# Performance work log

Hardware: AMD Instinct MI355X
Metric: run time of the kernel (lower is better)

Reference implementation:

```python
import jax, jax.numpy as jnp
import numpy as np

B, T, L, E, H, QS = 8, 8, 197, 768, 12, 16
C = E // H


def setup_inputs() -> dict:
    key = jax.random.key(0)
    ks = jax.random.split(key, 10)
    return dict(
        x=jax.random.normal(ks[0], (B, T, L, E), jnp.float32) * 0.02,
        s=jax.random.normal(ks[1], (B, QS, E), jnp.float32) * 0.02,
        te=jax.random.normal(ks[2], (T, E), jnp.float32) * 0.02,
        patch_mask=jax.random.normal(ks[3], (B, T, 1, L - 1, 1), jnp.float32) * 0.02,
        in_proj_weight=jax.random.normal(ks[4], (3 * E, E), jnp.float32) * 0.02,
        in_proj_bias=jax.random.normal(ks[5], (3 * E,), jnp.float32) * 0.02,
        out_w=jax.random.normal(ks[6], (E, E), jnp.float32) * 0.02,
        out_b=jax.random.normal(ks[7], (E,), jnp.float32) * 0.02,
        conv_w=jax.random.normal(ks[8], (E, 1, 3), jnp.float32) * 0.001,  # depthwise, groups=E
        conv_b=jax.random.normal(ks[9], (E,), jnp.float32) * 0.02,
    )


def _qkv(z, w, b, head_shape):
    # F.linear(z, w, b).chunk(3, -1), each reshaped to (*head_shape, H, C)
    zz = z @ w.T + b
    q, k, v = jnp.split(zz, 3, axis=-1)
    return (q.reshape(*head_shape, H, C),
            k.reshape(*head_shape, H, C),
            v.reshape(*head_shape, H, C))


def reference(x, s, te, patch_mask, in_proj_weight, in_proj_bias, out_w, out_b, conv_w, conv_b):
    scale = 1.0 / jnp.sqrt(jnp.asarray(C, x.dtype))

    # main self-attention over patches, per frame
    q, k, v = _qkv(x, in_proj_weight, in_proj_bias, (B, T, L))
    aff = jnp.einsum('ntqhc,ntkhc->ntqkh', q * scale, k)
    aff = jax.nn.softmax(aff, axis=-2)  # softmax over key dim (dim=-2)
    mix = jnp.einsum('ntqlh,ntlhc->ntqhc', aff, v)
    out = mix.reshape(B, T, L, E) @ out_w.T + out_b

    # syno cross-attention stream
    s_q, s_k, s_v = _qkv(s, in_proj_weight, in_proj_bias, (B, QS))
    te_q, te_k, te_v = _qkv(te, in_proj_weight, in_proj_bias, (T, 1))  # [T,1,H,C]
    _k = k[:, :, 1:]  # drop CLS -> [B,T,L-1,H,C]
    _v = v[:, :, 1:]
    s_aff = jnp.einsum('nqhc,ntkhc->ntqkh', s_q * scale, _k + te_k)
    s_aff = s_aff + patch_mask
    s_aff = jax.nn.softmax(s_aff, axis=-2)
    s_mix = jnp.einsum('ntqlh,ntlhc->ntqhc', s_aff, _v + te_v)  # [B,T,QS,H,C]

    # depthwise temporal conv (kernel 3, pad 1, groups=E) with residual
    sm = s_mix.transpose(0, 2, 3, 4, 1).reshape(B * QS, E, T)  # [N*Q, E, T]
    conv = jax.lax.conv_general_dilated(
        sm, conv_w, window_strides=(1,), padding=((1, 1),),
        feature_group_count=E, dimension_numbers=('NCH', 'OIH', 'NCH'))
    sm = conv + conv_b[None, :, None] + sm
    s_mix = sm.reshape(B, QS, H, C, T).transpose(0, 4, 1, 2, 3)  # [B,T,QS,H,C]

    s_mix = s_mix.mean(axis=1)  # mean over frames -> [B,QS,H,C]
    s_out = s_mix.reshape(B, QS, E) @ out_w.T + out_b

    return (q, k, v, out, s_q, s_k, s_v, s_out)
```

## Files before the change

### kernel.cpp

```cpp
#include <hip/hip_runtime.h>
#include <math.h>

constexpr int Bb  = 8;
constexpr int Tt  = 8;
constexpr int Ll  = 197;
constexpr int Ee  = 768;
constexpr int Hh  = 12;
constexpr int QSs = 16;
constexpr int Cc  = 64;
constexpr int MX    = Bb * Tt * Ll;
constexpr int MS    = Bb * QSs;
constexpr int MTE   = Tt;
constexpr int MALL  = MX + MS + MTE;
constexpr int MPAD  = 12800;
constexpr int KkP = 224;

using f32x4 = __attribute__((ext_vector_type(4))) float;
using s16x8 = __attribute__((ext_vector_type(8))) short;

__device__ __forceinline__ unsigned short f2bf(float f) {
    unsigned int u = __float_as_uint(f);
    u = (u + 0x7fffu + ((u >> 16) & 1u)) >> 16;
    return (unsigned short)u;
}

__global__ __launch_bounds__(256) void convert_all(
    const float* __restrict__ x, const float* __restrict__ s,
    const float* __restrict__ te, const float* __restrict__ ipw,
    const float* __restrict__ ow, unsigned short* __restrict__ xb,
    unsigned short* __restrict__ wb, unsigned short* __restrict__ owb)
{
    const long oX  = (long)MX * Ee;
    const long oS  = oX + (long)MS * Ee;
    const long oTe = oS + (long)MTE * Ee;
    const long nXp = (long)MPAD * Ee;
    const long nW  = (long)3 * Ee * Ee;
    const long nOW = (long)Ee * Ee;
    const long i4 = ((long)blockIdx.x * 256 + threadIdx.x) * 4;

    const float* src = nullptr; unsigned short* dst; long off, soff = 0;
    if (i4 < nXp) {
        dst = xb; off = i4;
        if      (off < oX)  { src = x;  soff = off; }
        else if (off < oS)  { src = s;  soff = off - oX; }
        else if (off < oTe) { src = te; soff = off - oS; }
    } else if (i4 < nXp + nW) {
        dst = wb; off = i4 - nXp; src = ipw; soff = off;
    } else if (i4 < nXp + nW + nOW) {
        dst = owb; off = i4 - nXp - nW; src = ow; soff = off;
    } else return;

    float4 v = make_float4(0.f, 0.f, 0.f, 0.f);
    if (src) v = *reinterpret_cast<const float4*>(src + soff);
    ushort4 o;
    o.x = f2bf(v.x); o.y = f2bf(v.y); o.z = f2bf(v.z); o.w = f2bf(v.w);
    *reinterpret_cast<ushort4*>(dst + off) = o;
}

struct DstPtrs { float* d[9]; };

__device__ __forceinline__ void load_lds16(const unsigned short* g, unsigned short* l) {
    __builtin_amdgcn_global_load_lds(
        (const __attribute__((address_space(1))) unsigned int*)g,
        (__attribute__((address_space(3))) unsigned int*)l,
        16, 0, 0);
}

__global__ __launch_bounds__(256) void mfma_gemm(
    const unsigned short* __restrict__ A,
    const unsigned short* __restrict__ W,
    const float* __restrict__ bias,
    DstPtrs dp, int Mmain, int Ms, int Mte,
    int ntiles, int tilesPerSeg)
{
    __shared__ __align__(16) unsigned short Asm[128 * 32];
    __shared__ __align__(16) unsigned short Bsm[128 * 32];

    const int nwg = gridDim.x;
    const int bid = blockIdx.x;
    const int q8 = nwg >> 3, r8 = nwg & 7;
    const int xcd = bid & 7, pos = bid >> 3;
    const int wgid = (xcd < r8 ? xcd * (q8 + 1)
                               : r8 * (q8 + 1) + (xcd - r8) * q8) + pos;
    const int mtile = wgid / ntiles;
    const int ntile = wgid - mtile * ntiles;

    const int tid  = threadIdx.x;
    const int wave = tid >> 6;
    const int lane = tid & 63;
    const int wr = wave >> 1, wc = wave & 1;
    const int m0  = mtile * 128;
    const int seg = ntile / tilesPerSeg;
    const int n0g = (ntile % tilesPerSeg) * 128;
    const int n0w = ntile * 128;

    f32x4 acc[4][4];
#pragma unroll
    for (int i = 0; i < 4; ++i)
#pragma unroll
        for (int j = 0; j < 4; ++j)
            acc[i][j] = f32x4{0.f, 0.f, 0.f, 0.f};

    const int srow = tid >> 2;
    const int scol = (tid & 3) * 8;
    unsigned short* ldsA = Asm + ((size_t)(tid >> 6)) * 512;
    unsigned short* ldsB = Bsm + ((size_t)(tid >> 6)) * 512;

    const int frow = lane & 15;
    const int fkc  = (lane >> 4) * 8;

    for (int k0 = 0; k0 < 768; k0 += 32) {
#pragma unroll
        for (int it = 0; it < 2; ++it) {
            const unsigned short* ga = A + (size_t)(m0 + srow + it * 64) * 768 + k0 + scol;
            const unsigned short* gb = W + (size_t)(n0w + srow + it * 64) * 768 + k0 + scol;
            load_lds16(ga, ldsA + it * 2048);
            load_lds16(gb, ldsB + it * 2048);
        }
        __syncthreads();

        s16x8 af[4], bf[4];
#pragma unroll
        for (int i = 0; i < 4; ++i) {
            const int ar = wr * 64 + i * 16 + frow;
            af[i] = *reinterpret_cast<const s16x8*>(&Asm[ar * 32 + fkc]);
        }
#pragma unroll
        for (int j = 0; j < 4; ++j) {
            const int br = wc * 64 + j * 16 + frow;
            bf[j] = *reinterpret_cast<const s16x8*>(&Bsm[br * 32 + fkc]);
        }
#pragma unroll
        for (int i = 0; i < 4; ++i)
#pragma unroll
            for (int j = 0; j < 4; ++j)
                acc[i][j] = __builtin_amdgcn_mfma_f32_16x16x32_bf16(
                    af[i], bf[j], acc[i][j], 0, 0, 0);
        __syncthreads();
    }

#pragma unroll
    for (int j = 0; j < 4; ++j) {
        const int col = wc * 64 + j * 16 + (lane & 15);
        const float bv = bias[n0w + col];
#pragma unroll
        for (int i = 0; i < 4; ++i) {
            const int gmBase = m0 + wr * 64 + i * 16 + ((lane >> 4) << 2);
            float* base; int lr;
            if (gmBase < Mmain)                { base = dp.d[seg];     lr = gmBase; }
            else if (gmBase < Mmain + Ms)      { base = dp.d[3 + seg]; lr = gmBase - Mmain; }
            else if (gmBase < Mmain + Ms + Mte){ base = dp.d[6 + seg]; lr = gmBase - Mmain - Ms; }
            else continue;
            float* p = base + (size_t)lr * 768 + n0g + col;
#pragma unroll
            for (int r = 0; r < 4; ++r)
                p[(size_t)r * 768] = acc[i][j][r] + bv;
        }
    }
}

__global__ __launch_bounds__(256) void attn_mfma(
    const float* __restrict__ q, const float* __restrict__ k,
    const float* __restrict__ v, unsigned short* __restrict__ mixb)
{
    __shared__ __align__(16) unsigned short Ks[KkP * 64];
    __shared__ __align__(16) unsigned short Vt[64 * 256];
    __shared__ __align__(16) unsigned short Pb[4 * 16 * 256];

    const int bidx = blockIdx.x;
    const int h  = bidx % Hh;
    const int bt = bidx / Hh;
    const int tid  = threadIdx.x;
    const int wave = tid >> 6;
    const int lane = tid & 63;
    const int l15  = lane & 15;
    const int g    = lane >> 4;
    const size_t gbase = (size_t)bt * Ll * Ee + (size_t)h * Cc;

    for (int idx = tid; idx < KkP * 16; idx += 256) {
        const int row = idx >> 4;
        const int cg  = idx & 15;
        float4 kv = make_float4(0.f, 0.f, 0.f, 0.f);
        if (row < Ll)
            kv = *reinterpret_cast<const float4*>(k + gbase + (size_t)row * Ee + cg * 4);
        ushort4 kb; kb.x = f2bf(kv.x); kb.y = f2bf(kv.y); kb.z = f2bf(kv.z); kb.w = f2bf(kv.w);
        const int kbyte = (row * 128 + cg * 8) ^ ((row & 7) << 4);
        *reinterpret_cast<ushort4*>((char*)Ks + kbyte) = kb;
    }
    for (int idx = tid; idx < 112 * 16; idx += 256) {
        const int rp = idx >> 4;
        const int cg = idx & 15;
        const int r0 = rp * 2, r1 = rp * 2 + 1;
        float4 v0 = make_float4(0.f, 0.f, 0.f, 0.f);
        float4 v1 = make_float4(0.f, 0.f, 0.f, 0.f);
        if (r0 < Ll) v0 = *reinterpret_cast<const float4*>(v + gbase + (size_t)r0 * Ee + cg * 4);
        if (r1 < Ll) v1 = *reinterpret_cast<const float4*>(v + gbase + (size_t)r1 * Ee + cg * 4);
        const float a0[4] = {v0.x, v0.y, v0.z, v0.w};
        const float a1[4] = {v1.x, v1.y, v1.z, v1.w};
#pragma unroll
        for (int i = 0; i < 4; ++i) {
            const int c = cg * 4 + i;
            const unsigned int w = (unsigned)f2bf(a0[i]) | ((unsigned)f2bf(a1[i]) << 16);
            const int vbyte = (c * 512 + rp * 4) ^ ((c & 7) << 4);
            *reinterpret_cast<unsigned int*>((char*)Vt + vbyte) = w;
        }
    }
    __syncthreads();

    char* Pw = (char*)(Pb + wave * 16 * 256);

    for (int qt = wave; qt < 13; qt += 4) {
        const int qrow = qt * 16 + l15;
        const float* qp = q + gbase + (size_t)qrow * Ee;
        s16x8 qf[2];
#pragma unroll
        for (int ks = 0; ks < 2; ++ks) {
            float4 a = make_float4(0.f, 0.f, 0.f, 0.f);
            float4 b = make_float4(0.f, 0.f, 0.f, 0.f);
            if (qrow < Ll) {
                a = *reinterpret_cast<const float4*>(qp + ks * 32 + g * 8);
                b = *reinterpret_cast<const float4*>(qp + ks * 32 + g * 8 + 4);
            }
            qf[ks] = s16x8{(short)f2bf(a.x), (short)f2bf(a.y), (short)f2bf(a.z), (short)f2bf(a.w),
                           (short)f2bf(b.x), (short)f2bf(b.y), (short)f2bf(b.z), (short)f2bf(b.w)};
        }

        float lsq = 0.f;
        for (int kt = 0; kt < 14; ++kt) {
            const int krow = kt * 16 + l15;
            f32x4 acc = {0.f, 0.f, 0.f, 0.f};
#pragma unroll
            for (int ks = 0; ks < 2; ++ks) {
                const int byte = (krow * 128 + ks * 64 + g * 16) ^ ((krow & 7) << 4);
                const s16x8 kf = *reinterpret_cast<const s16x8*>((const char*)Ks + byte);
                acc = __builtin_amdgcn_mfma_f32_16x16x32_bf16(kf, qf[ks], acc, 0, 0, 0);
            }
            float p[4];
#pragma unroll
            for (int r = 0; r < 4; ++r) {
                const int kg = kt * 16 + g * 4 + r;
                p[r] = (kg < Ll) ? __expf(acc[r] * 0.125f) : 0.f;
                lsq += p[r];
            }
            const unsigned int w0 = (unsigned)f2bf(p[0]) | ((unsigned)f2bf(p[1]) << 16);
            const unsigned int w1 = (unsigned)f2bf(p[2]) | ((unsigned)f2bf(p[3]) << 16);
            const int k0 = kt * 16 + g * 4;
            const int pbyte = (l15 * 512 + k0 * 2) ^ ((l15 & 7) << 4);
            *reinterpret_cast<unsigned int*>(Pw + pbyte)     = w0;
            *reinterpret_cast<unsigned int*>(Pw + pbyte + 4) = w1;
        }
        lsq += __shfl_xor(lsq, 16);
        lsq += __shfl_xor(lsq, 32);
        const float invl = 1.f / lsq;

#pragma unroll
        for (int ct = 0; ct < 4; ++ct) {
            f32x4 acc = {0.f, 0.f, 0.f, 0.f};
#pragma unroll
            for (int ks = 0; ks < 7; ++ks) {
                const int pbyte = (l15 * 512 + ks * 64 + g * 16) ^ ((l15 & 7) << 4);
                const s16x8 pf = *reinterpret_cast<const s16x8*>(Pw + pbyte);
                const int crow = ct * 16 + l15;
                const int vbyte = (crow * 512 + ks * 64 + g * 16) ^ ((crow & 7) << 4);
                const s16x8 vf = *reinterpret_cast<const s16x8*>((const char*)Vt + vbyte);
                acc = __builtin_amdgcn_mfma_f32_16x16x32_bf16(pf, vf, acc, 0, 0, 0);
            }
#pragma unroll
            for (int r = 0; r < 4; ++r) {
                const int qw = g * 4 + r;
                const float iv = __shfl(invl, qw);
                const int qg = qt * 16 + qw;
                if (qg < Ll) {
                    mixb[(size_t)(bt * Ll + qg) * Ee + h * Cc + ct * 16 + l15] =
                        f2bf(acc[r] * iv);
                }
            }
        }
    }
}

__global__ __launch_bounds__(256) void s_attn_v3(
    const float* __restrict__ sq, const float* __restrict__ k,
    const float* __restrict__ v, const float* __restrict__ tek,
    const float* __restrict__ tev, const float* __restrict__ pmask,
    float* __restrict__ smix)
{
    __shared__ float Ks[196][68];
    __shared__ float P[16][200];
    __shared__ float pm[196];
    __shared__ float teks[64];

    const int bt = blockIdx.x;
    const int h  = blockIdx.y;
    const int b  = bt / Tt;
    const int tt = bt % Tt;
    const int tid = threadIdx.x;
    const int qi = tid >> 4;
    const int kl = tid & 15;

    const size_t kbase = (size_t)bt * Ll * Ee + (size_t)h * Cc;
    for (int idx = tid; idx < 196 * 16; idx += 256) {
        const int row = idx >> 4;
        const int cg  = (idx & 15) * 4;
        *reinterpret_cast<float4*>(&Ks[row][cg]) =
            *reinterpret_cast<const float4*>(k + kbase + (size_t)(row + 1) * Ee + cg);
    }
    if (tid < 64) teks[tid] = tek[tt * Ee + h * Cc + tid];
    for (int i = tid; i < 196; i += 256)
        pm[i] = pmask[(size_t)bt * 196 + i];
    __syncthreads();

    float qr[Cc];
    const size_t sqbase = ((size_t)(b * QSs + qi)) * Ee + (size_t)h * Cc;
#pragma unroll
    for (int c4 = 0; c4 < 16; ++c4) {
        const float4 qv = *reinterpret_cast<const float4*>(sq + sqbase + c4 * 4);
        qr[c4*4+0] = qv.x; qr[c4*4+1] = qv.y; qr[c4*4+2] = qv.z; qr[c4*4+3] = qv.w;
    }
    float qte = 0.f;
#pragma unroll
    for (int c = 0; c < Cc; ++c) qte += qr[c] * teks[c];

    float lsum = 0.f;
    for (int i = 0; i < 13; ++i) {
        const int kk = kl + 16 * i;
        if (kk < 196) {
            float d = 0.f;
#pragma unroll
            for (int c4 = 0; c4 < 16; ++c4) {
                const float4 kv = *reinterpret_cast<const float4*>(&Ks[kk][c4 * 4]);
                d += qr[c4*4+0]*kv.x + qr[c4*4+1]*kv.y + qr[c4*4+2]*kv.z + qr[c4*4+3]*kv.w;
            }
            const float p = __expf((d + qte) * 0.125f + pm[kk]);
            P[qi][kk] = p;
            lsum += p;
        }
    }
    lsum += __shfl_xor(lsum, 1);
    lsum += __shfl_xor(lsum, 2);
    lsum += __shfl_xor(lsum, 4);
    lsum += __shfl_xor(lsum, 8);
    const float invl = 1.f / lsum;
    __syncthreads();

    const int c = kl * 4;
    const float4 tv = *reinterpret_cast<const float4*>(tev + tt * Ee + h * Cc + c);
    float a0 = 0.f, a1 = 0.f, a2 = 0.f, a3 = 0.f;
    const float* vbase = v + kbase + Ee + c;
    for (int kk = 0; kk < 196; ++kk) {
        const float p = P[qi][kk];
        const float4 vv = *reinterpret_cast<const float4*>(vbase + (size_t)kk * Ee);
        a0 += p * vv.x; a1 += p * vv.y; a2 += p * vv.z; a3 += p * vv.w;
    }
    float4 o;
    o.x = a0 * invl + tv.x; o.y = a1 * invl + tv.y;
    o.z = a2 * invl + tv.z; o.w = a3 * invl + tv.w;
    *reinterpret_cast<float4*>(
        smix + ((size_t)(bt * QSs + qi)) * Ee + (size_t)h * Cc + c) = o;
}

__global__ __launch_bounds__(256) void conv_mean_kernel(
    const float* __restrict__ smix, const float* __restrict__ cw,
    const float* __restrict__ cb, unsigned short* __restrict__ meansm_b)
{
    const int idx = blockIdx.x * 256 + threadIdx.x;
    if (idx >= Bb * QSs * Ee) return;
    const int e  = idx % Ee;
    const int n  = idx / Ee;
    const int b  = n / QSs;
    const int qi = n % QSs;

    float v0 = 0.f, vlast = 0.f, S = 0.f;
#pragma unroll
    for (int t = 0; t < Tt; ++t) {
        const float val = smix[((size_t)(b * Tt + t) * QSs + qi) * Ee + e];
        if (t == 0) v0 = val;
        if (t == Tt - 1) vlast = val;
        S += val;
    }
    const float w0 = cw[e * 3 + 0], w1 = cw[e * 3 + 1], w2 = cw[e * 3 + 2];
    const float tot = S + w0 * (S - vlast) + w1 * S + w2 * (S - v0);
    meansm_b[idx] = f2bf(tot * (1.f / Tt) + cb[e]);
}

extern "C" void kernel_launch(void* const* d_in, const int* in_sizes, int n_in,
                              void* d_out, int out_size, void* d_ws, size_t ws_size,
                              hipStream_t stream)
{
    const float* x     = (const float*)d_in[0];
    const float* s     = (const float*)d_in[1];
    const float* te    = (const float*)d_in[2];
    const float* pmask = (const float*)d_in[3];
    const float* ipw   = (const float*)d_in[4];
    const float* ipb   = (const float*)d_in[5];
    const float* ow    = (const float*)d_in[6];
    const float* ob    = (const float*)d_in[7];
    const float* cw    = (const float*)d_in[8];
    const float* cb    = (const float*)d_in[9];

    float* out = (float*)d_out;
    const size_t NX = (size_t)MX;
    float* q_o    = out;
    float* k_o    = q_o  + NX * Ee;
    float* v_o    = k_o  + NX * Ee;
    float* out_o  = v_o  + NX * Ee;
    float* sq_o   = out_o + NX * Ee;
    float* sk_o   = sq_o + (size_t)MS * Ee;
    float* sv_o   = sk_o + (size_t)MS * Ee;
    float* sout_o = sv_o + (size_t)MS * Ee;

    char* wsb = (char*)d_ws;
    unsigned short* xb   = (unsigned short*)wsb;
    unsigned short* wb   = xb + (size_t)MPAD * Ee;
    unsigned short* owb  = wb + (size_t)3 * Ee * Ee;
    unsigned short* meansm_b = owb + (size_t)Ee * Ee;
    float* teq    = (float*)(meansm_b + (size_t)MS * Ee);
    float* tek    = teq + (size_t)MTE * Ee;
    float* tev    = tek + (size_t)MTE * Ee;
    float* smix   = tev + (size_t)MTE * Ee;
    unsigned short* mixb = xb;

    const long nXp = (long)MPAD * Ee;
    const long nW  = (long)3 * Ee * Ee;
    const long nOW = (long)Ee * Ee;
    const long nCvt = (nXp + nW + nOW) / 4;

    convert_all<<<dim3((nCvt + 255) / 256), 256, 0, stream>>>(
        x, s, te, ipw, ow, xb, wb, owb);

    {
        DstPtrs dp;
        dp.d[0] = q_o;  dp.d[1] = k_o;  dp.d[2] = v_o;
        dp.d[3] = sq_o; dp.d[4] = sk_o; dp.d[5] = sv_o;
        dp.d[6] = teq;  dp.d[7] = tek;  dp.d[8] = tev;
        mfma_gemm<<<dim3((MPAD / 128) * 18), 256, 0, stream>>>(
            xb, wb, ipb, dp, MX, MS, MTE, 18, 6);
    }

    attn_mfma<<<dim3(Bb * Tt * Hh), 256, 0, stream>>>(q_o, k_o, v_o, mixb);

    {
        DstPtrs dp;
        dp.d[0] = out_o; dp.d[1] = out_o; dp.d[2] = out_o;
        for (int i = 3; i < 9; ++i) dp.d[i] = out_o;
        mfma_gemm<<<dim3(99 * 6), 256, 0, stream>>>(
            mixb, owb, ob, dp, MX, 0, 0, 6, 6);
    }

    s_attn_v3<<<dim3(Bb * Tt, Hh), 256, 0, stream>>>(
        sq_o, k_o, v_o, tek, tev, pmask, smix);

    conv_mean_kernel<<<dim3((Bb * QSs * Ee + 255) / 256), 256, 0, stream>>>(
        smix, cw, cb, meansm_b);

    {
        DstPtrs dp;
        for (int i = 0; i < 9; ++i) dp.d[i] = sout_o;
        mfma_gemm<<<dim3(6), 256, 0, stream>>>(
            meansm_b, owb, ob, dp, MS, 0, 0, 6, 6);
    }
}
```

Baseline: 251.1 us.

## Double-buffer LDS tiles in MFMA GEMM to overlap global loads with compute

Splits the A and B shared-memory tiles into two buffers and prefetches the next K-slice through direct global-to-LDS loads while MFMAs run on the current slice. This aims to hide global load latency that previously stalled at the barrier each iteration. It doubles LDS use per block, which may lower occupancy, and adds an explicit vmcnt wait before every barrier.

```diff
diff --git a/kernel.cpp b/kernel.cpp
--- a/kernel.cpp
+++ b/kernel.cpp
@@ -73,8 +73,8 @@
     DstPtrs dp, int Mmain, int Ms, int Mte,
     int ntiles, int tilesPerSeg)
 {
-    __shared__ __align__(16) unsigned short Asm[128 * 32];
-    __shared__ __align__(16) unsigned short Bsm[128 * 32];
+    __shared__ __align__(16) unsigned short Asm[2][128 * 32];
+    __shared__ __align__(16) unsigned short Bsm[2][128 * 32];
 
     const int nwg = gridDim.x;
     const int bid = blockIdx.x;
@@ -103,32 +103,43 @@
 
     const int srow = tid >> 2;
     const int scol = (tid & 3) * 8;
-    unsigned short* ldsA = Asm + ((size_t)(tid >> 6)) * 512;
-    unsigned short* ldsB = Bsm + ((size_t)(tid >> 6)) * 512;
+    const int woff = wave * 512;
 
     const int frow = lane & 15;
     const int fkc  = (lane >> 4) * 8;
 
-    for (int k0 = 0; k0 < 768; k0 += 32) {
-#pragma unroll
-        for (int it = 0; it < 2; ++it) {
-            const unsigned short* ga = A + (size_t)(m0 + srow + it * 64) * 768 + k0 + scol;
-            const unsigned short* gb = W + (size_t)(n0w + srow + it * 64) * 768 + k0 + scol;
-            load_lds16(ga, ldsA + it * 2048);
-            load_lds16(gb, ldsB + it * 2048);
-        }
-        __syncthreads();
+    const unsigned short* gA = A + (size_t)(m0 + srow) * 768 + scol;
+    const unsigned short* gB = W + (size_t)(n0w + srow) * 768 + scol;
+
+#pragma unroll
+    for (int it = 0; it < 2; ++it) {
+        load_lds16(gA + (size_t)it * 64 * 768, &Asm[0][woff + it * 2048]);
+        load_lds16(gB + (size_t)it * 64 * 768, &Bsm[0][woff + it * 2048]);
+    }
+    asm volatile("s_waitcnt vmcnt(0)" ::: "memory");
+    __syncthreads();
+
+    for (int t = 0; t < 24; ++t) {
+        const int cur = t & 1;
+        if (t < 23) {
+            const int k1 = (t + 1) * 32;
+#pragma unroll
+            for (int it = 0; it < 2; ++it) {
+                load_lds16(gA + k1 + (size_t)it * 64 * 768, &Asm[cur ^ 1][woff + it * 2048]);
+                load_lds16(gB + k1 + (size_t)it * 64 * 768, &Bsm[cur ^ 1][woff + it * 2048]);
+            }
+        }
 
         s16x8 af[4], bf[4];
 #pragma unroll
         for (int i = 0; i < 4; ++i) {
             const int ar = wr * 64 + i * 16 + frow;
-            af[i] = *reinterpret_cast<const s16x8*>(&Asm[ar * 32 + fkc]);
+            af[i] = *reinterpret_cast<const s16x8*>(&Asm[cur][ar * 32 + fkc]);
         }
 #pragma unroll
         for (int j = 0; j < 4; ++j) {
             const int br = wc * 64 + j * 16 + frow;
-            bf[j] = *reinterpret_cast<const s16x8*>(&Bsm[br * 32 + fkc]);
+            bf[j] = *reinterpret_cast<const s16x8*>(&Bsm[cur][br * 32 + fkc]);
         }
 #pragma unroll
         for (int i = 0; i < 4; ++i)
@@ -136,6 +147,8 @@
             for (int j = 0; j < 4; ++j)
                 acc[i][j] = __builtin_amdgcn_mfma_f32_16x16x32_bf16(
                     af[i], bf[j], acc[i][j], 0, 0, 0);
+
+        asm volatile("s_waitcnt vmcnt(0)" ::: "memory");
         __syncthreads();
     }
 
```

Result: no change. 256.1 us (+2.0%).

## Triple-buffer LDS tiles in QKV GEMM to overlap global loads with MFMA

Applied to the files above, without the earlier changes.

Moves the bf16 GEMM main loop from single-buffered LDS with two barriers per k-step to a three-stage ring. Loads for tile k+2 are issued before computing tile k, with partial vmcnt waits and one barrier per step. It also raises wave priority around the MFMA block. This hides global-to-LDS latency behind compute, at the cost of three times the LDS footprint, which could lower occupancy, and a fragile hand-written waitcnt scheme.

```diff
diff --git a/kernel.cpp b/kernel.cpp
--- a/kernel.cpp
+++ b/kernel.cpp
@@ -73,8 +73,8 @@
     DstPtrs dp, int Mmain, int Ms, int Mte,
     int ntiles, int tilesPerSeg)
 {
-    __shared__ __align__(16) unsigned short Asm[128 * 32];
-    __shared__ __align__(16) unsigned short Bsm[128 * 32];
+    __shared__ __align__(16) unsigned short Asm[3][128 * 32];
+    __shared__ __align__(16) unsigned short Bsm[3][128 * 32];
 
     const int nwg = gridDim.x;
     const int bid = blockIdx.x;
@@ -103,41 +103,69 @@
 
     const int srow = tid >> 2;
     const int scol = (tid & 3) * 8;
-    unsigned short* ldsA = Asm + ((size_t)(tid >> 6)) * 512;
-    unsigned short* ldsB = Bsm + ((size_t)(tid >> 6)) * 512;
+    const int woff = wave * 512;
 
     const int frow = lane & 15;
     const int fkc  = (lane >> 4) * 8;
 
-    for (int k0 = 0; k0 < 768; k0 += 32) {
-#pragma unroll
-        for (int it = 0; it < 2; ++it) {
-            const unsigned short* ga = A + (size_t)(m0 + srow + it * 64) * 768 + k0 + scol;
-            const unsigned short* gb = W + (size_t)(n0w + srow + it * 64) * 768 + k0 + scol;
-            load_lds16(ga, ldsA + it * 2048);
-            load_lds16(gb, ldsB + it * 2048);
-        }
-        __syncthreads();
-
+    const unsigned short* gA = A + (size_t)(m0 + srow) * 768 + scol;
+    const unsigned short* gB = W + (size_t)(n0w + srow) * 768 + scol;
+
+    auto STAGE = [&](int kt, int buf) {
+        const int k1 = kt * 32;
+        load_lds16(gA + k1,                        &Asm[buf][woff]);
+        load_lds16(gA + k1 + (size_t)64 * 768,     &Asm[buf][woff + 2048]);
+        load_lds16(gB + k1,                        &Bsm[buf][woff]);
+        load_lds16(gB + k1 + (size_t)64 * 768,     &Bsm[buf][woff + 2048]);
+    };
+
+    auto COMPUTE = [&](int buf) {
         s16x8 af[4], bf[4];
 #pragma unroll
         for (int i = 0; i < 4; ++i) {
             const int ar = wr * 64 + i * 16 + frow;
-            af[i] = *reinterpret_cast<const s16x8*>(&Asm[ar * 32 + fkc]);
+            af[i] = *reinterpret_cast<const s16x8*>(&Asm[buf][ar * 32 + fkc]);
         }
 #pragma unroll
         for (int j = 0; j < 4; ++j) {
             const int br = wc * 64 + j * 16 + frow;
-            bf[j] = *reinterpret_cast<const s16x8*>(&Bsm[br * 32 + fkc]);
-        }
+            bf[j] = *reinterpret_cast<const s16x8*>(&Bsm[buf][br * 32 + fkc]);
+        }
+        __builtin_amdgcn_s_setprio(1);
 #pragma unroll
         for (int i = 0; i < 4; ++i)
 #pragma unroll
             for (int j = 0; j < 4; ++j)
                 acc[i][j] = __builtin_amdgcn_mfma_f32_16x16x32_bf16(
                     af[i], bf[j], acc[i][j], 0, 0, 0);
-        __syncthreads();
-    }
+        __builtin_amdgcn_s_setprio(0);
+    };
+
+    STAGE(0, 0);
+    STAGE(1, 1);
+    __builtin_amdgcn_sched_barrier(0);
+    asm volatile("s_waitcnt vmcnt(4)" ::: "memory");
+    __builtin_amdgcn_s_barrier();
+    __builtin_amdgcn_sched_barrier(0);
+
+    int cur = 0;
+    for (int t = 0; t < 22; ++t) {
+        const int nxt2 = (cur >= 1) ? cur - 1 : cur + 2;
+        STAGE(t + 2, nxt2);
+        COMPUTE(cur);
+        __builtin_amdgcn_sched_barrier(0);
+        asm volatile("s_waitcnt vmcnt(4)" ::: "memory");
+        __builtin_amdgcn_s_barrier();
+        __builtin_amdgcn_sched_barrier(0);
+        cur = (cur >= 2) ? 0 : cur + 1;
+    }
+    COMPUTE(cur);
+    __builtin_amdgcn_sched_barrier(0);
+    asm volatile("s_waitcnt vmcnt(0)" ::: "memory");
+    __builtin_amdgcn_s_barrier();
+    __builtin_amdgcn_sched_barrier(0);
+    cur = (cur >= 2) ? 0 : cur + 1;
+    COMPUTE(cur);
 
 #pragma unroll
     for (int j = 0; j < 4; ++j) {
```

Result: no change. 255.0 us (+1.6%).
